# Optimization experiments

Hardware: AMD Instinct MI355X
Metric: run time of the kernel (lower is better)

The kernel has to match this reference:

```python
import jax, jax.numpy as jnp
import numpy as np

U = 100000  # num_users
I = 100000  # num_items
D = 64      # dims
L = 50      # seq_L


def setup_inputs() -> dict:
    key = jax.random.key(0)
    ks = jax.random.split(key, 12)
    B, T = 4096, 100
    inp = {
        "user_ids": jax.random.randint(ks[0], (B,), 0, U),
        "item_seq_ids": jax.random.randint(ks[1], (B, L), 0, I),
        "target_item_ids": jax.random.randint(ks[2], (B, T), 0, I),
        # embedding tables (normal init)
        "user_table": jax.random.normal(ks[3], (U, D), jnp.float32) * 0.01,
        "item_table": jax.random.normal(ks[4], (I, D), jnp.float32) * 0.01,
        "W2_table": jax.random.normal(ks[5], (I, D), jnp.float32) * 0.01,
        "b2_table": jnp.zeros((I, 1), jnp.float32),
        # feature gates: Linear(dims, dims), he_uniform weight, zero bias
        "fg_item_W": jax.random.uniform(ks[6], (D, D), jnp.float32, -1.0, 1.0) * np.sqrt(6.0 / D),
        "fg_item_b": jnp.zeros((D,), jnp.float32),
        "fg_user_W": jax.random.uniform(ks[7], (D, D), jnp.float32, -1.0, 1.0) * np.sqrt(6.0 / D),
        "fg_user_b": jnp.zeros((D,), jnp.float32),
        # instance gates: xavier_uniform
        "inst_gate_item": jax.random.uniform(ks[8], (D, 1), jnp.float32, -1.0, 1.0) * np.sqrt(6.0 / (D + 1)),
        "inst_gate_user": jax.random.uniform(ks[9], (D, L), jnp.float32, -1.0, 1.0) * np.sqrt(6.0 / (D + L)),
    }
    return inp


def _forward_user(user_emb, item_embs, fg_item_W, fg_item_b, fg_user_W, fg_user_b,
                  inst_gate_item, inst_gate_user):
    # user_emb: [B,D], item_embs: [B,L,D]
    gate = jax.nn.sigmoid(
        item_embs @ fg_item_W.T + fg_item_b
        + (user_emb @ fg_user_W.T + fg_user_b)[:, None, :]
    )  # [B,L,D]
    gated = item_embs * gate  # [B,L,D]
    term1 = jnp.einsum("bld,d->bl", gated, inst_gate_item[:, 0])
    term2 = user_emb @ inst_gate_user  # [B,L]
    inst = jax.nn.sigmoid(term1 + term2)  # [B,L]
    union = jnp.sum(gated * inst[:, :, None], axis=1)  # [B,D]
    union = union / jnp.sum(inst, axis=1, keepdims=True)
    return union


def reference(user_ids, item_seq_ids, target_item_ids, user_table, item_table,
              W2_table, b2_table, fg_item_W, fg_item_b, fg_user_W, fg_user_b,
              inst_gate_item, inst_gate_user):
    item_embs = item_table[item_seq_ids]      # [B,L,D]
    user_emb = user_table[user_ids]           # [B,D]
    union = _forward_user(user_emb, item_embs, fg_item_W, fg_item_b,
                          fg_user_W, fg_user_b, inst_gate_item, inst_gate_user)
    w2 = W2_table[target_item_ids]            # [B,T,D]
    b2 = b2_table[target_item_ids][..., 0]    # [B,T]
    res = b2 + jnp.einsum("btd,bd->bt", w2, user_emb)
    res = res + jnp.einsum("bd,btd->bt", union, w2)
    # rel_score: bmm(item_embs, w2^T) summed over L == contract item_embs summed over L with w2
    res = res + jnp.einsum("bd,btd->bt", jnp.sum(item_embs, axis=1), w2)
    return res
```

## Files before the change

kernel.cpp:

```cpp
#include <hip/hip_runtime.h>

#define DD 64
#define LL 50
#define NB 4096
#define NT 100

typedef __attribute__((ext_vector_type(8))) __bf16 bf16x8;
typedef __attribute__((ext_vector_type(4))) float f32x4;

__device__ __forceinline__ float sigmoidf_(float x) {
    return 1.0f / (1.0f + __expf(-x));
}
__device__ __forceinline__ unsigned pack_bf16(float hi, float lo) {
    union { float f; unsigned u; } a, b;
    a.f = hi; b.f = lo;
    return ((a.u + 0x8000u) & 0xffff0000u) | ((b.u + 0x8000u) >> 16);
}
__device__ __forceinline__ uint4 cvt8u(const float* f) {
    uint4 r;
    r.x = pack_bf16(f[1], f[0]);
    r.y = pack_bf16(f[3], f[2]);
    r.z = pack_bf16(f[5], f[4]);
    r.w = pack_bf16(f[7], f[6]);
    return r;
}
__device__ __forceinline__ bf16x8 cvt8(const float* f) {
    return __builtin_bit_cast(bf16x8, cvt8u(f));
}
__device__ __forceinline__ void glds16(const float* g, float* l) {
    __builtin_amdgcn_global_load_lds(
        (const __attribute__((address_space(1))) void*)g,
        (__attribute__((address_space(3))) void*)l, 16, 0, 0);
}
__device__ __forceinline__ void glds4(const float* g, float* l) {
    __builtin_amdgcn_global_load_lds(
        (const __attribute__((address_space(1))) void*)g,
        (__attribute__((address_space(3))) void*)l, 4, 0, 0);
}

__global__ __launch_bounds__(128) void k0_user(
    const int* __restrict__ uid_g, const float* __restrict__ user_table,
    const float* __restrict__ Wu, const float* __restrict__ bu,
    const float* __restrict__ bi, const float* __restrict__ igu,
    const float* __restrict__ Wi,
    float* __restrict__ ufg_ws, float* __restrict__ t2_ws,
    unsigned short* __restrict__ wiB_ws)
{
    if (blockIdx.x == 256) {
        if (threadIdx.x >= 64) return;
        const int n = threadIdx.x;
        float tmp[64];
#pragma unroll
        for (int c4 = 0; c4 < 16; c4++)
            *(float4*)&tmp[c4 * 4] = *(const float4*)(Wi + n * DD + c4 * 4);
#pragma unroll
        for (int ch = 0; ch < 8; ch++)
            *(uint4*)(wiB_ws + n * DD + ch * 8) = cvt8u(tmp + ch * 8);
        return;
    }

    const int lane = threadIdx.x & 63;
    const int wv = threadIdx.x >> 6;
    const int c = lane & 15, q = lane >> 4;
    const int uid = uid_g[blockIdx.x * 16 + c];
    const float* urow = user_table + (size_t)uid * DD;

    bf16x8 af[2];
#pragma unroll
    for (int kf = 0; kf < 2; kf++) {
        float tmp[8];
        *(float4*)&tmp[0] = *(const float4*)(urow + kf * 32 + q * 8);
        *(float4*)&tmp[4] = *(const float4*)(urow + kf * 32 + q * 8 + 4);
        af[kf] = cvt8(tmp);
    }

#pragma unroll
    for (int ni0 = 0; ni0 < 4; ni0++) {
        const int ni = wv * 4 + ni0;
        f32x4 a = {0.f, 0.f, 0.f, 0.f};
#pragma unroll
        for (int kf = 0; kf < 2; kf++) {
            const int k0 = kf * 32 + q * 8;
            float tmp[8];
            if (ni < 4) {
                const float* src = Wu + (ni * 16 + c) * DD + k0;
                *(float4*)&tmp[0] = *(const float4*)src;
                *(float4*)&tmp[4] = *(const float4*)(src + 4);
            } else {
                const int l = ni * 16 + c - 64;
#pragma unroll
                for (int j = 0; j < 8; j++)
                    tmp[j] = (l < LL) ? igu[(k0 + j) * LL + l] : 0.f;
            }
            a = __builtin_amdgcn_mfma_f32_16x16x32_bf16(af[kf], cvt8(tmp), a, 0, 0, 0);
        }
        const int n = ni * 16 + c;
#pragma unroll
        for (int reg = 0; reg < 4; reg++) {
            const int bo = blockIdx.x * 16 + q * 4 + reg;
            if (n < DD)           ufg_ws[bo * DD + n] = a[reg] + bu[n] + bi[n];
            else if (n < DD + LL) t2_ws[bo * DD + (n - DD)] = a[reg];
        }
    }
}

__global__ __launch_bounds__(256) void k1_fused(
    const int* __restrict__ uid_g, const int* __restrict__ iid_g,
    const int* __restrict__ tgt_g,
    const float* __restrict__ user_table, const float* __restrict__ item_table,
    const float* __restrict__ W2, const float* __restrict__ b2,
    const unsigned short* __restrict__ wiB, const float* __restrict__ igi,
    const float* __restrict__ ufg_ws, const float* __restrict__ t2_ws,
    float* __restrict__ out)
{
    const int tid = threadIdx.x;
    const int lane = tid & 63;
    const int w = tid >> 6;
    const int c = lane & 15, q = lane >> 4;
    const int b = blockIdx.x;

    __shared__ __align__(16) float sE[52 * DD];
    __shared__ __align__(16) float sW[112 * DD];
    __shared__ __align__(16) float sT[DD];
    __shared__ __align__(16) float sB[128];
    __shared__ __align__(16) float sU[4 * DD];
    __shared__ __align__(16) float sS[4 * DD];
    __shared__ float sI[4];
    __shared__ __align__(16) float sV[DD];
    __shared__ float sOut[112];

    const int* iidp = iid_g + b * LL;
    const int* tgtp = tgt_g + b * NT;

    int iid3[3];
#pragma unroll
    for (int k = 0; k < 3; k++) {
        const int s = w + 4 * k;
        const int r = 4 * s + (lane >> 4);
        iid3[k] = iidp[r < LL ? r : LL - 1];
    }
    int iid12 = 0;
    if (w == 0) {
        const int r = 48 + (lane >> 4);
        iid12 = iidp[r < LL ? r : LL - 1];
    }
#pragma unroll
    for (int k = 0; k < 3; k++) {
        const int s = w + 4 * k;
        const int r = 4 * s + (lane >> 4);
        const int j2 = (lane & 15) ^ (r & 7);
        glds16(item_table + (size_t)iid3[k] * DD + j2 * 4, sE + s * 256);
    }
    if (w == 0) {
        const int r = 48 + (lane >> 4);
        const int j2 = (lane & 15) ^ (r & 7);
        glds16(item_table + (size_t)iid12 * DD + j2 * 4, sE + 12 * 256);
    }

    int tids6[6];
#pragma unroll
    for (int i = 0; i < 6; i++) {
        const int s2 = w + 4 * i;
        tids6[i] = tgtp[4 * s2 + (lane >> 4)];
    }
    int tid24 = 0;
    if (w == 0) tid24 = tgtp[96 + (lane >> 4)];
#pragma unroll
    for (int i = 0; i < 6; i++) {
        const int s2 = w + 4 * i;
        glds16(W2 + (size_t)tids6[i] * DD + (lane & 15) * 4, sW + s2 * 256);
    }
    if (w == 0)
        glds16(W2 + (size_t)tid24 * DD + (lane & 15) * 4, sW + 24 * 256);

    if (w < 2) {
        const int sl = w * 64 + lane;
        const int tb = sl < NT ? sl : NT - 1;
        glds4(b2 + tgtp[tb], sB + w * 64);
    }
    if (w == 1)
        glds4(t2_ws + b * DD + (lane < LL ? lane : LL - 1), sT);

    bf16x8 wb[4][2];
#pragma unroll
    for (int ni = 0; ni < 4; ni++)
#pragma unroll
        for (int kf = 0; kf < 2; kf++)
            wb[ni][kf] = __builtin_bit_cast(bf16x8,
                *(const uint4*)(wiB + (ni * 16 + c) * DD + kf * 32 + q * 8));

    float ufg4[4], igi4[4];
#pragma unroll
    for (int ni = 0; ni < 4; ni++) {
        ufg4[ni] = ufg_ws[b * DD + ni * 16 + c];
        igi4[ni] = igi[ni * 16 + c];
    }
    float u = 0.f;
    if (w == 0) {
        const int uid = uid_g[b];
        u = user_table[(size_t)uid * DD + lane];
    }

    __syncthreads();

    bf16x8 ea[2];
    {
        const int row = w * 16 + c;
        const int rr = (row < LL) ? row : 0;
        const float* rowp = sE + rr * DD;
        const int s7 = rr & 7;
#pragma unroll
        for (int kf = 0; kf < 2; kf++) {
            float tmp[8];
            const int ch0 = (kf * 8 + 2 * q) ^ s7;
            const int ch1 = (kf * 8 + 2 * q + 1) ^ s7;
            *(float4*)&tmp[0] = *(const float4*)(rowp + ch0 * 4);
            *(float4*)&tmp[4] = *(const float4*)(rowp + ch1 * 4);
            if (row >= LL) {
#pragma unroll
                for (int i = 0; i < 8; i++) tmp[i] = 0.f;
            }
            ea[kf] = cvt8(tmp);
        }
    }

    float unum[4] = {0.f, 0.f, 0.f, 0.f};
    float sip[4]  = {0.f, 0.f, 0.f, 0.f};
    float isum = 0.f;
    {
        f32x4 acc[4];
#pragma unroll
        for (int ni = 0; ni < 4; ni++) {
            f32x4 a = {0.f, 0.f, 0.f, 0.f};
            a = __builtin_amdgcn_mfma_f32_16x16x32_bf16(ea[0], wb[ni][0], a, 0, 0, 0);
            a = __builtin_amdgcn_mfma_f32_16x16x32_bf16(ea[1], wb[ni][1], a, 0, 0, 0);
            acc[ni] = a;
        }
        float gated[4][4], inst_r[4];
#pragma unroll
        for (int reg = 0; reg < 4; reg++) {
            const int l = w * 16 + q * 4 + reg;
            const int valid = (l < LL);
            const int lr = valid ? l : 0;
            const int s7 = lr & 7;
            float t1 = 0.f;
#pragma unroll
            for (int ni = 0; ni < 4; ni++) {
                const int phys = (4 * ni + (c >> 2)) ^ s7;
                const float ev = sE[lr * DD + phys * 4 + (c & 3)];
                const float e = valid ? ev : 0.f;
                const float g = sigmoidf_(acc[ni][reg] + ufg4[ni]);
                const float gd = e * g;
                gated[reg][ni] = gd;
                t1 += gd * igi4[ni];
                sip[ni] += e;
            }
            t1 += __shfl_xor(t1, 1); t1 += __shfl_xor(t1, 2);
            t1 += __shfl_xor(t1, 4); t1 += __shfl_xor(t1, 8);
            inst_r[reg] = valid ? sigmoidf_(t1 + sT[lr]) : 0.f;
        }
#pragma unroll
        for (int reg = 0; reg < 4; reg++) {
            isum += inst_r[reg];
#pragma unroll
            for (int ni = 0; ni < 4; ni++)
                unum[ni] += gated[reg][ni] * inst_r[reg];
        }
    }

#pragma unroll
    for (int ni = 0; ni < 4; ni++) {
        unum[ni] += __shfl_xor(unum[ni], 16); unum[ni] += __shfl_xor(unum[ni], 32);
        sip[ni]  += __shfl_xor(sip[ni], 16);  sip[ni]  += __shfl_xor(sip[ni], 32);
    }
    isum += __shfl_xor(isum, 16); isum += __shfl_xor(isum, 32);

    const float un = (q == 0) ? unum[0] : (q == 1) ? unum[1] : (q == 2) ? unum[2] : unum[3];
    const float si = (q == 0) ? sip[0]  : (q == 1) ? sip[1]  : (q == 2) ? sip[2]  : sip[3];
    sU[w * DD + lane] = un;
    sS[w * DD + lane] = si;
    if (lane == 0) sI[w] = isum;
    __syncthreads();

    if (w == 0) {
        const float unt = sU[lane] + sU[DD + lane] + sU[2 * DD + lane] + sU[3 * DD + lane];
        const float sit = sS[lane] + sS[DD + lane] + sS[2 * DD + lane] + sS[3 * DD + lane];
        const float ist = sI[0] + sI[1] + sI[2] + sI[3];
        sV[lane] = u + unt / ist + sit;
    }
    __syncthreads();

    const int j = tid & 15, gg = tid >> 4;
    const float4 vr = *(const float4*)&sV[j * 4];
#pragma unroll
    for (int i = 0; i < 7; i++) {
        const int ts = i * 16 + gg;
        const float4 wvv = *(const float4*)&sW[ts * DD + j * 4];
        float s = wvv.x * vr.x + wvv.y * vr.y + wvv.z * vr.z + wvv.w * vr.w;
        s += __shfl_xor(s, 1); s += __shfl_xor(s, 2);
        s += __shfl_xor(s, 4); s += __shfl_xor(s, 8);
        if (j == 0 && ts < NT) sOut[ts] = s + sB[ts];
    }
    __syncthreads();
    if (tid < NT) out[b * NT + tid] = sOut[tid];
}

extern "C" void kernel_launch(void* const* d_in, const int* in_sizes, int n_in,
                              void* d_out, int out_size, void* d_ws, size_t ws_size,
                              hipStream_t stream)
{
    const int* user_ids        = (const int*)d_in[0];
    const int* item_seq_ids    = (const int*)d_in[1];
    const int* target_item_ids = (const int*)d_in[2];
    const float* user_tab      = (const float*)d_in[3];
    const float* item_tab      = (const float*)d_in[4];
    const float* W2_tab        = (const float*)d_in[5];
    const float* b2_tab        = (const float*)d_in[6];
    const float* fg_item_W     = (const float*)d_in[7];
    const float* fg_item_b     = (const float*)d_in[8];
    const float* fg_user_W     = (const float*)d_in[9];
    const float* fg_user_b     = (const float*)d_in[10];
    const float* igi           = (const float*)d_in[11];
    const float* igu           = (const float*)d_in[12];
    float* out = (float*)d_out;

    float* ufg_ws = (float*)d_ws;
    float* t2_ws  = ufg_ws + NB * DD;
    unsigned short* wiB_ws = (unsigned short*)(t2_ws + NB * DD);

    k0_user<<<257, 128, 0, stream>>>(user_ids, user_tab, fg_user_W, fg_user_b,
                                     fg_item_b, igu, fg_item_W,
                                     ufg_ws, t2_ws, wiB_ws);
    k1_fused<<<NB, 256, 0, stream>>>(user_ids, item_seq_ids, target_item_ids,
                                     user_tab, item_tab, W2_tab, b2_tab,
                                     wiB_ws, igi, ufg_ws, t2_ws, out);
}
```

Baseline: 167.9 us.

## Load W2 rows into registers, drop a barrier, use hardware rcp and bf16 pack

W2 target rows are now loaded straight into registers (float4 per thread) instead of staged through a 28KB LDS buffer. This cuts LDS use and can raise occupancy, which the launch bounds now request at 4 blocks per SM. The user embedding moves to async LDS loads, and the final vector reduction is done by every thread, which removes one barrier. It also uses the hardware reciprocal for sigmoid and the division, and a packed bf16 convert instruction. The cost is higher register pressure from holding 7 float4s across the gate computation, and slightly lower precision from rcp and round-to-nearest pack differences.

```diff
diff --git a/kernel.cpp b/kernel.cpp
--- a/kernel.cpp
+++ b/kernel.cpp
@@ -9,7 +9,7 @@
 typedef __attribute__((ext_vector_type(4))) float f32x4;
 
 __device__ __forceinline__ float sigmoidf_(float x) {
-    return 1.0f / (1.0f + __expf(-x));
+    return __builtin_amdgcn_rcpf(1.0f + __expf(-x));
 }
 __device__ __forceinline__ unsigned pack_bf16(float hi, float lo) {
     union { float f; unsigned u; } a, b;
@@ -26,6 +26,19 @@
 }
 __device__ __forceinline__ bf16x8 cvt8(const float* f) {
     return __builtin_bit_cast(bf16x8, cvt8u(f));
+}
+__device__ __forceinline__ unsigned cvtpk(float lo, float hi) {
+    unsigned r;
+    asm("v_cvt_pk_bf16_f32 %0, %1, %2" : "=v"(r) : "v"(lo), "v"(hi));
+    return r;
+}
+__device__ __forceinline__ bf16x8 cvt8f(const float* f) {
+    uint4 r;
+    r.x = cvtpk(f[0], f[1]);
+    r.y = cvtpk(f[2], f[3]);
+    r.z = cvtpk(f[4], f[5]);
+    r.w = cvtpk(f[6], f[7]);
+    return __builtin_bit_cast(bf16x8, r);
 }
 __device__ __forceinline__ void glds16(const float* g, float* l) {
     __builtin_amdgcn_global_load_lds(
@@ -104,7 +117,7 @@
     }
 }
 
-__global__ __launch_bounds__(256) void k1_fused(
+__global__ __launch_bounds__(256, 4) void k1_fused(
     const int* __restrict__ uid_g, const int* __restrict__ iid_g,
     const int* __restrict__ tgt_g,
     const float* __restrict__ user_table, const float* __restrict__ item_table,
@@ -117,16 +130,16 @@
     const int lane = tid & 63;
     const int w = tid >> 6;
     const int c = lane & 15, q = lane >> 4;
+    const int j = tid & 15, gg = tid >> 4;
     const int b = blockIdx.x;
 
     __shared__ __align__(16) float sE[52 * DD];
-    __shared__ __align__(16) float sW[112 * DD];
     __shared__ __align__(16) float sT[DD];
     __shared__ __align__(16) float sB[128];
     __shared__ __align__(16) float sU[4 * DD];
     __shared__ __align__(16) float sS[4 * DD];
+    __shared__ __align__(16) float sUu[DD];
     __shared__ float sI[4];
-    __shared__ __align__(16) float sV[DD];
     __shared__ float sOut[112];
 
     const int* iidp = iid_g + b * LL;
@@ -157,29 +170,39 @@
         glds16(item_table + (size_t)iid12 * DD + j2 * 4, sE + 12 * 256);
     }
 
-    int tids6[6];
-#pragma unroll
-    for (int i = 0; i < 6; i++) {
-        const int s2 = w + 4 * i;
-        tids6[i] = tgtp[4 * s2 + (lane >> 4)];
-    }
-    int tid24 = 0;
-    if (w == 0) tid24 = tgtp[96 + (lane >> 4)];
-#pragma unroll
-    for (int i = 0; i < 6; i++) {
-        const int s2 = w + 4 * i;
-        glds16(W2 + (size_t)tids6[i] * DD + (lane & 15) * 4, sW + s2 * 256);
-    }
-    if (w == 0)
-        glds16(W2 + (size_t)tid24 * DD + (lane & 15) * 4, sW + 24 * 256);
-
-    if (w < 2) {
-        const int sl = w * 64 + lane;
-        const int tb = sl < NT ? sl : NT - 1;
-        glds4(b2 + tgtp[tb], sB + w * 64);
-    }
     if (w == 1)
         glds4(t2_ws + b * DD + (lane < LL ? lane : LL - 1), sT);
+    if (w == 2) {
+        const int tb = lane < NT ? lane : NT - 1;
+        glds4(b2 + tgtp[tb], sB);
+        const int uid = uid_g[b];
+        glds4(user_table + (size_t)uid * DD + lane, sUu);
+    }
+    if (w == 3) {
+        const int sl = 64 + lane;
+        const int tb = sl < NT ? sl : NT - 1;
+        glds4(b2 + tgtp[tb], sB + 64);
+    }
+
+    int tt[7];
+#pragma unroll
+    for (int i = 0; i < 7; i++) {
+        const int ts = i * 16 + gg;
+        tt[i] = tgtp[ts < NT ? ts : NT - 1];
+    }
+    float4 wv[7];
+#pragma unroll
+    for (int i = 0; i < 7; i++)
+        wv[i] = *(const float4*)(W2 + (size_t)tt[i] * DD + j * 4);
+
+    float ufg4[4], igi4[4];
+#pragma unroll
+    for (int ni = 0; ni < 4; ni++) {
+        ufg4[ni] = ufg_ws[b * DD + ni * 16 + c];
+        igi4[ni] = igi[ni * 16 + c];
+    }
+
+    __syncthreads();
 
     bf16x8 wb[4][2];
 #pragma unroll
@@ -188,20 +211,6 @@
         for (int kf = 0; kf < 2; kf++)
             wb[ni][kf] = __builtin_bit_cast(bf16x8,
                 *(const uint4*)(wiB + (ni * 16 + c) * DD + kf * 32 + q * 8));
-
-    float ufg4[4], igi4[4];
-#pragma unroll
-    for (int ni = 0; ni < 4; ni++) {
-        ufg4[ni] = ufg_ws[b * DD + ni * 16 + c];
-        igi4[ni] = igi[ni * 16 + c];
-    }
-    float u = 0.f;
-    if (w == 0) {
-        const int uid = uid_g[b];
-        u = user_table[(size_t)uid * DD + lane];
-    }
-
-    __syncthreads();
 
     bf16x8 ea[2];
     {
@@ -220,7 +229,7 @@
 #pragma unroll
                 for (int i = 0; i < 8; i++) tmp[i] = 0.f;
             }
-            ea[kf] = cvt8(tmp);
+            ea[kf] = cvt8f(tmp);
         }
     }
 
@@ -236,13 +245,13 @@
             a = __builtin_amdgcn_mfma_f32_16x16x32_bf16(ea[1], wb[ni][1], a, 0, 0, 0);
             acc[ni] = a;
         }
-        float gated[4][4], inst_r[4];
 #pragma unroll
         for (int reg = 0; reg < 4; reg++) {
             const int l = w * 16 + q * 4 + reg;
             const int valid = (l < LL);
             const int lr = valid ? l : 0;
             const int s7 = lr & 7;
+            float gd[4];
             float t1 = 0.f;
 #pragma unroll
             for (int ni = 0; ni < 4; ni++) {
@@ -250,21 +259,17 @@
                 const float ev = sE[lr * DD + phys * 4 + (c & 3)];
                 const float e = valid ? ev : 0.f;
                 const float g = sigmoidf_(acc[ni][reg] + ufg4[ni]);
-                const float gd = e * g;
-                gated[reg][ni] = gd;
-                t1 += gd * igi4[ni];
+                gd[ni] = e * g;
+                t1 += gd[ni] * igi4[ni];
                 sip[ni] += e;
             }
             t1 += __shfl_xor(t1, 1); t1 += __shfl_xor(t1, 2);
             t1 += __shfl_xor(t1, 4); t1 += __shfl_xor(t1, 8);
-            inst_r[reg] = valid ? sigmoidf_(t1 + sT[lr]) : 0.f;
-        }
-#pragma unroll
-        for (int reg = 0; reg < 4; reg++) {
-            isum += inst_r[reg];
+            const float inst = valid ? sigmoidf_(t1 + sT[lr]) : 0.f;
+            isum += inst;
 #pragma unroll
             for (int ni = 0; ni < 4; ni++)
-                unum[ni] += gated[reg][ni] * inst_r[reg];
+                unum[ni] += gd[ni] * inst;
         }
     }
 
@@ -282,21 +287,28 @@
     if (lane == 0) sI[w] = isum;
     __syncthreads();
 
-    if (w == 0) {
-        const float unt = sU[lane] + sU[DD + lane] + sU[2 * DD + lane] + sU[3 * DD + lane];
-        const float sit = sS[lane] + sS[DD + lane] + sS[2 * DD + lane] + sS[3 * DD + lane];
-        const float ist = sI[0] + sI[1] + sI[2] + sI[3];
-        sV[lane] = u + unt / ist + sit;
-    }
-    __syncthreads();
-
-    const int j = tid & 15, gg = tid >> 4;
-    const float4 vr = *(const float4*)&sV[j * 4];
+    float4 vr;
+    {
+        const float4 u0 = *(const float4*)&sU[0 * DD + j * 4];
+        const float4 u1 = *(const float4*)&sU[1 * DD + j * 4];
+        const float4 u2 = *(const float4*)&sU[2 * DD + j * 4];
+        const float4 u3 = *(const float4*)&sU[3 * DD + j * 4];
+        const float4 s0 = *(const float4*)&sS[0 * DD + j * 4];
+        const float4 s1 = *(const float4*)&sS[1 * DD + j * 4];
+        const float4 s2 = *(const float4*)&sS[2 * DD + j * 4];
+        const float4 s3 = *(const float4*)&sS[3 * DD + j * 4];
+        const float4 uu = *(const float4*)&sUu[j * 4];
+        const float rist = __builtin_amdgcn_rcpf(sI[0] + sI[1] + sI[2] + sI[3]);
+        vr.x = uu.x + (u0.x + u1.x + u2.x + u3.x) * rist + (s0.x + s1.x + s2.x + s3.x);
+        vr.y = uu.y + (u0.y + u1.y + u2.y + u3.y) * rist + (s0.y + s1.y + s2.y + s3.y);
+        vr.z = uu.z + (u0.z + u1.z + u2.z + u3.z) * rist + (s0.z + s1.z + s2.z + s3.z);
+        vr.w = uu.w + (u0.w + u1.w + u2.w + u3.w) * rist + (s0.w + s1.w + s2.w + s3.w);
+    }
+
 #pragma unroll
     for (int i = 0; i < 7; i++) {
         const int ts = i * 16 + gg;
-        const float4 wvv = *(const float4*)&sW[ts * DD + j * 4];
-        float s = wvv.x * vr.x + wvv.y * vr.y + wvv.z * vr.z + wvv.w * vr.w;
+        float s = wv[i].x * vr.x + wv[i].y * vr.y + wv[i].z * vr.z + wv[i].w * vr.w;
         s += __shfl_xor(s, 1); s += __shfl_xor(s, 2);
         s += __shfl_xor(s, 4); s += __shfl_xor(s, 8);
         if (j == 0 && ts < NT) sOut[ts] = s + sB[ts];
```

Measured after the change: 154.6 us. 1.09x faster.
